# Optimization experiments

Hardware: AMD Instinct MI355X
Metric: run time of the kernel (lower is better)

Reference implementation:

```python
import jax, jax.numpy as jnp
import numpy as np

NUM_HEADS = 16
EPS = 1e-6


def _phi(x):
    # Positive feature map: ELU + 1
    return jax.nn.elu(x) + 1.0


def setup_inputs() -> dict:
    key = jax.random.key(0)
    ks = jax.random.split(key, 5)
    B, L, D = 4, 8192, 1024
    scale = 0.02
    return {
        "x": jax.random.normal(ks[0], (B, L, D), dtype=jnp.float32),
        "Wq": jax.random.normal(ks[1], (D, D), dtype=jnp.float32) * scale,
        "Wk": jax.random.normal(ks[2], (D, D), dtype=jnp.float32) * scale,
        "Wv": jax.random.normal(ks[3], (D, D), dtype=jnp.float32) * scale,
        "Wo": jax.random.normal(ks[4], (D, D), dtype=jnp.float32) * scale,
    }


def reference(x, Wq, Wk, Wv, Wo):
    B, L, D = x.shape
    H = NUM_HEADS
    dh = D // H
    # Projections (bias-free linear layers)
    Q = x @ Wq
    K = x @ Wk
    V = x @ Wv
    # Split heads: (B, H, L, dh)
    Qh = Q.reshape(B, L, H, dh).transpose(0, 2, 1, 3)
    Kh = K.reshape(B, L, H, dh).transpose(0, 2, 1, 3)
    Vh = V.reshape(B, L, H, dh).transpose(0, 2, 1, 3)
    Qf = _phi(Qh)
    Kf = _phi(Kh)
    # Global key-value reduction over time: (B, H, dh, dh)
    Kv = jnp.einsum('bhlm,bhln->bhmn', Kf, Vh)
    # Key normalizer: (B, H, dh)
    K1 = jnp.sum(Kf, axis=2)
    # Numerator / denominator
    num = jnp.einsum('bhlm,bhmn->bhln', Qf, Kv)
    den = jnp.einsum('bhlm,bhm->bhl', Qf, K1) + EPS
    out = num / den[..., None]
    out = out.transpose(0, 2, 1, 3).reshape(B, L, D)
    return out @ Wo
```

## Files before the change

### kernel.cpp

```cpp
#include <hip/hip_runtime.h>
#include <stdint.h>
#include <stddef.h>

typedef __bf16 bf16;
typedef __attribute__((ext_vector_type(8))) __bf16 bf16x8;
typedef __attribute__((ext_vector_type(4))) __bf16 bf16x4;
typedef __attribute__((ext_vector_type(4))) float f32x4;

#define ATT_EPS 1e-6f

__device__ __forceinline__ void lds16(const void* g, void* l) {
    __builtin_amdgcn_global_load_lds(
        (const __attribute__((address_space(1))) void*)g,
        (__attribute__((address_space(3))) void*)l, 16, 0, 0);
}

__global__ __launch_bounds__(256) void cvt_bf16(const float4* __restrict__ in,
                                                bf16x4* __restrict__ out, int n4) {
    int i = blockIdx.x * 256 + threadIdx.x;
    if (i < n4) {
        float4 v = in[i];
        bf16x4 o;
        o.x = (bf16)v.x; o.y = (bf16)v.y; o.z = (bf16)v.z; o.w = (bf16)v.w;
        out[i] = o;
    }
}

__global__ __launch_bounds__(256) void transpose_w(const float* __restrict__ W,
                                                   bf16* __restrict__ Wt) {
    __shared__ float tile[32][33];
    const int bx = blockIdx.x * 32, by = blockIdx.y * 32;
    const int tx = threadIdx.x, ty = threadIdx.y;
#pragma unroll
    for (int j = 0; j < 32; j += 8)
        tile[ty + j][tx] = W[(size_t)(by + ty + j) * 1024 + bx + tx];
    __syncthreads();
#pragma unroll
    for (int j = 0; j < 32; j += 8)
        Wt[(size_t)(bx + ty + j) * 1024 + by + tx] = (bf16)tile[tx][ty + j];
}

template <int MODE>
__global__ __launch_bounds__(256) void gemm_bt(const bf16* __restrict__ A, int lda,
                                               const bf16* __restrict__ B, int ldb,
                                               void* __restrict__ C, int ldc, int K) {
    __shared__ bf16 sA[128 * 32] __attribute__((aligned(16)));
    __shared__ bf16 sB[128 * 32] __attribute__((aligned(16)));
    const int t = threadIdx.x;
    const int wave = t >> 6;
    const int lane = t & 63;
    const int tileM = blockIdx.y * 128;
    const int tileN = blockIdx.x * 128;
    const int wm = (wave >> 1) * 64;
    const int wn = (wave & 1) * 64;

    f32x4 acc[4][4] = {};

    const int srow = t >> 2;
    const int scol = (t & 3) * 8;
    const bf16* a0 = A + (size_t)(tileM + srow) * lda + scol;
    const bf16* a1 = A + (size_t)(tileM + 64 + srow) * lda + scol;
    const bf16* b0 = B + (size_t)(tileN + srow) * ldb + scol;
    const bf16* b1 = B + (size_t)(tileN + 64 + srow) * ldb + scol;
    bf16* dA0 = sA + wave * 512;
    bf16* dA1 = sA + 2048 + wave * 512;
    bf16* dB0 = sB + wave * 512;
    bf16* dB1 = sB + 2048 + wave * 512;

    const int rm = lane & 15;
    const int qk = (lane >> 4) * 8;

    for (int k0 = 0; k0 < K; k0 += 32) {
        lds16(a0 + k0, dA0);
        lds16(a1 + k0, dA1);
        lds16(b0 + k0, dB0);
        lds16(b1 + k0, dB1);
        __builtin_amdgcn_s_waitcnt(0);
        __syncthreads();
        bf16x8 af[4], bfr[4];
#pragma unroll
        for (int mi = 0; mi < 4; mi++)
            af[mi] = *(const bf16x8*)&sA[(wm + mi * 16 + rm) * 32 + qk];
#pragma unroll
        for (int ni = 0; ni < 4; ni++)
            bfr[ni] = *(const bf16x8*)&sB[(wn + ni * 16 + rm) * 32 + qk];
#pragma unroll
        for (int mi = 0; mi < 4; mi++)
#pragma unroll
            for (int ni = 0; ni < 4; ni++)
                acc[mi][ni] = __builtin_amdgcn_mfma_f32_16x16x32_bf16(
                    af[mi], bfr[ni], acc[mi][ni], 0, 0, 0);
        __syncthreads();
    }

    const int row0 = (lane >> 4) * 4;
    const int col = lane & 15;
#pragma unroll
    for (int mi = 0; mi < 4; mi++) {
#pragma unroll
        for (int ni = 0; ni < 4; ni++) {
#pragma unroll
            for (int r = 0; r < 4; r++) {
                int gm = tileM + wm + mi * 16 + row0 + r;
                int gn = tileN + wn + ni * 16 + col;
                float v = acc[mi][ni][r];
                if (MODE == 2) v = (v > 0.f) ? (v + 1.f) : __expf(v);
                if (MODE == 0)
                    ((float*)C)[(size_t)gm * ldc + gn] = v;
                else
                    ((bf16*)C)[(size_t)gm * ldc + gn] = (bf16)v;
            }
        }
    }
}

__global__ __launch_bounds__(256) void kv_reduce(const bf16* __restrict__ Kft,
                                                 const bf16* __restrict__ Vt,
                                                 float* __restrict__ Kv) {
    const int chunk = blockIdx.x;
    const int bh = blockIdx.y;
    const int b = bh >> 4, h = bh & 15;
    __shared__ bf16 sA[64 * 32] __attribute__((aligned(16)));
    __shared__ bf16 sB[64 * 32] __attribute__((aligned(16)));
    const int t = threadIdx.x, wave = t >> 6, lane = t & 63;
    const size_t cbase = (size_t)b * 8192 + (size_t)chunk * 2048;
    const int srow = t >> 2, scol = (t & 3) * 8;
    const bf16* a0 = Kft + (size_t)(h * 64 + srow) * 32768 + cbase + scol;
    const bf16* b0 = Vt + (size_t)(h * 64 + srow) * 32768 + cbase + scol;
    bf16* dA = sA + wave * 512;
    bf16* dB = sB + wave * 512;
    const int rm = lane & 15, qk = (lane >> 4) * 8;

    f32x4 acc[4] = {};
    f32x4 acc1 = {0.f, 0.f, 0.f, 0.f};
    bf16x8 ones;
#pragma unroll
    for (int j = 0; j < 8; j++) ones[j] = (bf16)1.0f;

    for (int k0 = 0; k0 < 2048; k0 += 32) {
        lds16(a0 + k0, dA);
        lds16(b0 + k0, dB);
        __builtin_amdgcn_s_waitcnt(0);
        __syncthreads();
        bf16x8 af = *(const bf16x8*)&sA[(wave * 16 + rm) * 32 + qk];
        bf16x8 bfr[4];
#pragma unroll
        for (int ni = 0; ni < 4; ni++)
            bfr[ni] = *(const bf16x8*)&sB[(ni * 16 + rm) * 32 + qk];
#pragma unroll
        for (int ni = 0; ni < 4; ni++)
            acc[ni] = __builtin_amdgcn_mfma_f32_16x16x32_bf16(af, bfr[ni], acc[ni], 0, 0, 0);
        acc1 = __builtin_amdgcn_mfma_f32_16x16x32_bf16(af, ones, acc1, 0, 0, 0);
        __syncthreads();
    }

    float* out = Kv + bh * 65 * 64;
    const int row0 = (lane >> 4) * 4, col = lane & 15;
    const int m0 = wave * 16 + row0;
#pragma unroll
    for (int ni = 0; ni < 4; ni++)
#pragma unroll
        for (int r = 0; r < 4; r++)
            atomicAdd(&out[(ni * 16 + col) * 64 + m0 + r], acc[ni][r]);
    if (col == 0) {
#pragma unroll
        for (int r = 0; r < 4; r++) atomicAdd(&out[64 * 64 + m0 + r], acc1[r]);
    }
}

__global__ __launch_bounds__(256) void attn_out(const bf16* __restrict__ Qf,
                                                const float* __restrict__ Kv,
                                                bf16* __restrict__ attn) {
    const int lt = blockIdx.x;
    const int bh = blockIdx.y;
    const int b = bh >> 4, h = bh & 15;
    __shared__ bf16 sQ[128 * 64] __attribute__((aligned(16)));
    __shared__ bf16 sB[80 * 64] __attribute__((aligned(16)));
    __shared__ float den[128];
    const int t = threadIdx.x, wave = t >> 6, lane = t & 63;
    const int qrow = t >> 3, qc = (t & 7) * 8;
    const bf16* qp = Qf + (size_t)(b * 8192 + lt * 128 + qrow) * 1024 + h * 64 + qc;
#pragma unroll
    for (int i = 0; i < 4; i++)
        lds16(qp + (size_t)i * 32 * 1024, sQ + i * 2048 + wave * 512);
    const float* kv = Kv + bh * 65 * 64;
    for (int idx = t; idx < 80 * 64; idx += 256) {
        int n = idx >> 6, k2 = idx & 63;
        sB[idx] = (n < 65) ? (bf16)kv[n * 64 + k2] : (bf16)0.f;
    }
    __builtin_amdgcn_s_waitcnt(0);
    __syncthreads();

    f32x4 acc[2][5] = {};
    const int rm = lane & 15, qk = (lane >> 4) * 8;
#pragma unroll
    for (int k0 = 0; k0 < 64; k0 += 32) {
        bf16x8 af[2], bfr[5];
#pragma unroll
        for (int mi = 0; mi < 2; mi++)
            af[mi] = *(const bf16x8*)&sQ[(wave * 32 + mi * 16 + rm) * 64 + k0 + qk];
#pragma unroll
        for (int ni = 0; ni < 5; ni++)
            bfr[ni] = *(const bf16x8*)&sB[(ni * 16 + rm) * 64 + k0 + qk];
#pragma unroll
        for (int mi = 0; mi < 2; mi++)
#pragma unroll
            for (int ni = 0; ni < 5; ni++)
                acc[mi][ni] = __builtin_amdgcn_mfma_f32_16x16x32_bf16(
                    af[mi], bfr[ni], acc[mi][ni], 0, 0, 0);
    }

    const int row0 = (lane >> 4) * 4, col = lane & 15;
    if (col == 0) {
#pragma unroll
        for (int mi = 0; mi < 2; mi++)
#pragma unroll
            for (int r = 0; r < 4; r++)
                den[wave * 32 + mi * 16 + row0 + r] = acc[mi][4][r] + ATT_EPS;
    }
    __syncthreads();
#pragma unroll
    for (int mi = 0; mi < 2; mi++) {
#pragma unroll
        for (int ni = 0; ni < 4; ni++) {
#pragma unroll
            for (int r = 0; r < 4; r++) {
                int rl = wave * 32 + mi * 16 + row0 + r;
                float v = acc[mi][ni][r] / den[rl];
                attn[(size_t)(b * 8192 + lt * 128 + rl) * 1024 + h * 64 + ni * 16 + col] =
                    (bf16)v;
            }
        }
    }
}

extern "C" void kernel_launch(void* const* d_in, const int* in_sizes, int n_in,
                              void* d_out, int out_size, void* d_ws, size_t ws_size,
                              hipStream_t stream) {
    const float* x  = (const float*)d_in[0];
    const float* Wq = (const float*)d_in[1];
    const float* Wk = (const float*)d_in[2];
    const float* Wv = (const float*)d_in[3];
    const float* Wo = (const float*)d_in[4];

    char* ws = (char*)d_ws;
    bf16* xb  = (bf16*)ws;
    bf16* Qf  = (bf16*)(ws + ((size_t)64 << 20));
    bf16* Kft = (bf16*)(ws + ((size_t)128 << 20));
    bf16* Vt  = (bf16*)(ws + ((size_t)192 << 20));
    bf16* Wqt = (bf16*)(ws + ((size_t)256 << 20));
    bf16* Wkt = Wqt + 1024 * 1024;
    bf16* Wvt = Wkt + 1024 * 1024;
    bf16* Wot = Wvt + 1024 * 1024;
    float* Kv = (float*)(Wot + 1024 * 1024);
    bf16* attn = xb;

    cvt_bf16<<<8388608 / 256, 256, 0, stream>>>((const float4*)x, (bf16x4*)xb, 8388608);
    dim3 tb(32, 8);
    transpose_w<<<dim3(32, 32), tb, 0, stream>>>(Wq, Wqt);
    transpose_w<<<dim3(32, 32), tb, 0, stream>>>(Wk, Wkt);
    transpose_w<<<dim3(32, 32), tb, 0, stream>>>(Wv, Wvt);
    transpose_w<<<dim3(32, 32), tb, 0, stream>>>(Wo, Wot);
    hipMemsetAsync(Kv, 0, (size_t)64 * 65 * 64 * sizeof(float), stream);

    gemm_bt<2><<<dim3(8, 256), 256, 0, stream>>>(xb, 1024, Wqt, 1024, Qf, 1024, 1024);
    gemm_bt<2><<<dim3(256, 8), 256, 0, stream>>>(Wkt, 1024, xb, 1024, Kft, 32768, 1024);
    gemm_bt<1><<<dim3(256, 8), 256, 0, stream>>>(Wvt, 1024, xb, 1024, Vt, 32768, 1024);
    kv_reduce<<<dim3(4, 64), 256, 0, stream>>>(Kft, Vt, Kv);
    attn_out<<<dim3(64, 64), 256, 0, stream>>>(Qf, Kv, attn);
    gemm_bt<0><<<dim3(8, 256), 256, 0, stream>>>(attn, 1024, Wot, 1024, d_out, 1024, 1024);
}
```

Baseline: 740.7 us.

## Fuse K and V projections into one GEMM and swizzle tile order

The separate K and V projection GEMMs are merged into a single kernel that loads each x tile once and computes both Wk·x and Wv·x accumulators, with the ELU+1 applied to K in the epilogue. This halves the reads of x for those projections. All GEMMs also switch to a 1D grid with a swizzled block-to-tile mapping, grouping 8 N-tiles per M-group for better L2 reuse. The fused kernel doubles the accumulator registers, so it uses launch_bounds(256,2) and 24KB of LDS, which may reduce occupancy or cause spills.

```diff
diff --git a/kernel.cpp b/kernel.cpp
--- a/kernel.cpp
+++ b/kernel.cpp
@@ -13,6 +13,11 @@
     __builtin_amdgcn_global_load_lds(
         (const __attribute__((address_space(1))) void*)g,
         (__attribute__((address_space(3))) void*)l, 16, 0, 0);
+}
+
+__device__ __forceinline__ void swizzle_uv(int lin, int& u, int& v) {
+    u = (lin & 7) | ((lin >> 6) << 3);
+    v = (lin >> 3) & 7;
 }
 
 __global__ __launch_bounds__(256) void cvt_bf16(const float4* __restrict__ in,
@@ -49,8 +54,10 @@
     const int t = threadIdx.x;
     const int wave = t >> 6;
     const int lane = t & 63;
-    const int tileM = blockIdx.y * 128;
-    const int tileN = blockIdx.x * 128;
+    int u, v;
+    swizzle_uv(blockIdx.x, u, v);
+    const int tileM = u * 128;
+    const int tileN = v * 128;
     const int wm = (wave >> 1) * 64;
     const int wn = (wave & 1) * 64;
 
@@ -103,12 +110,100 @@
             for (int r = 0; r < 4; r++) {
                 int gm = tileM + wm + mi * 16 + row0 + r;
                 int gn = tileN + wn + ni * 16 + col;
-                float v = acc[mi][ni][r];
-                if (MODE == 2) v = (v > 0.f) ? (v + 1.f) : __expf(v);
+                float val = acc[mi][ni][r];
+                if (MODE == 2) val = (val > 0.f) ? (val + 1.f) : __expf(val);
                 if (MODE == 0)
-                    ((float*)C)[(size_t)gm * ldc + gn] = v;
+                    ((float*)C)[(size_t)gm * ldc + gn] = val;
                 else
-                    ((bf16*)C)[(size_t)gm * ldc + gn] = (bf16)v;
+                    ((bf16*)C)[(size_t)gm * ldc + gn] = (bf16)val;
+            }
+        }
+    }
+}
+
+__global__ __launch_bounds__(256, 2) void kv_proj(const bf16* __restrict__ Wkt,
+                                                  const bf16* __restrict__ Wvt,
+                                                  const bf16* __restrict__ xb,
+                                                  bf16* __restrict__ Kft,
+                                                  bf16* __restrict__ Vt) {
+    __shared__ bf16 sK[128 * 32] __attribute__((aligned(16)));
+    __shared__ bf16 sV[128 * 32] __attribute__((aligned(16)));
+    __shared__ bf16 sX[128 * 32] __attribute__((aligned(16)));
+    const int t = threadIdx.x;
+    const int wave = t >> 6;
+    const int lane = t & 63;
+    int u, v;
+    swizzle_uv(blockIdx.x, u, v);
+    const int tileM = v * 128;
+    const int tileN = u * 128;
+    const int wm = (wave >> 1) * 64;
+    const int wn = (wave & 1) * 64;
+
+    f32x4 accK[4][4] = {};
+    f32x4 accV[4][4] = {};
+
+    const int srow = t >> 2;
+    const int scol = (t & 3) * 8;
+    const bf16* k0p = Wkt + (size_t)(tileM + srow) * 1024 + scol;
+    const bf16* k1p = k0p + (size_t)64 * 1024;
+    const bf16* v0p = Wvt + (size_t)(tileM + srow) * 1024 + scol;
+    const bf16* v1p = v0p + (size_t)64 * 1024;
+    const bf16* x0p = xb + (size_t)(tileN + srow) * 1024 + scol;
+    const bf16* x1p = x0p + (size_t)64 * 1024;
+    bf16* dK0 = sK + wave * 512;
+    bf16* dK1 = sK + 2048 + wave * 512;
+    bf16* dV0 = sV + wave * 512;
+    bf16* dV1 = sV + 2048 + wave * 512;
+    bf16* dX0 = sX + wave * 512;
+    bf16* dX1 = sX + 2048 + wave * 512;
+
+    const int rm = lane & 15;
+    const int qk = (lane >> 4) * 8;
+
+    for (int k0 = 0; k0 < 1024; k0 += 32) {
+        lds16(k0p + k0, dK0);
+        lds16(k1p + k0, dK1);
+        lds16(v0p + k0, dV0);
+        lds16(v1p + k0, dV1);
+        lds16(x0p + k0, dX0);
+        lds16(x1p + k0, dX1);
+        __builtin_amdgcn_s_waitcnt(0);
+        __syncthreads();
+        bf16x8 bfr[4], afK[4], afV[4];
+#pragma unroll
+        for (int ni = 0; ni < 4; ni++)
+            bfr[ni] = *(const bf16x8*)&sX[(wn + ni * 16 + rm) * 32 + qk];
+#pragma unroll
+        for (int mi = 0; mi < 4; mi++) {
+            afK[mi] = *(const bf16x8*)&sK[(wm + mi * 16 + rm) * 32 + qk];
+            afV[mi] = *(const bf16x8*)&sV[(wm + mi * 16 + rm) * 32 + qk];
+        }
+#pragma unroll
+        for (int mi = 0; mi < 4; mi++)
+#pragma unroll
+            for (int ni = 0; ni < 4; ni++) {
+                accK[mi][ni] = __builtin_amdgcn_mfma_f32_16x16x32_bf16(
+                    afK[mi], bfr[ni], accK[mi][ni], 0, 0, 0);
+                accV[mi][ni] = __builtin_amdgcn_mfma_f32_16x16x32_bf16(
+                    afV[mi], bfr[ni], accV[mi][ni], 0, 0, 0);
+            }
+        __syncthreads();
+    }
+
+    const int row0 = (lane >> 4) * 4;
+    const int col = lane & 15;
+#pragma unroll
+    for (int mi = 0; mi < 4; mi++) {
+#pragma unroll
+        for (int ni = 0; ni < 4; ni++) {
+#pragma unroll
+            for (int r = 0; r < 4; r++) {
+                int gm = tileM + wm + mi * 16 + row0 + r;
+                int gn = tileN + wn + ni * 16 + col;
+                float kv_ = accK[mi][ni][r];
+                kv_ = (kv_ > 0.f) ? (kv_ + 1.f) : __expf(kv_);
+                Kft[(size_t)gm * 32768 + gn] = (bf16)kv_;
+                Vt[(size_t)gm * 32768 + gn] = (bf16)accV[mi][ni][r];
             }
         }
     }
@@ -226,9 +321,9 @@
 #pragma unroll
             for (int r = 0; r < 4; r++) {
                 int rl = wave * 32 + mi * 16 + row0 + r;
-                float v = acc[mi][ni][r] / den[rl];
+                float vv = acc[mi][ni][r] / den[rl];
                 attn[(size_t)(b * 8192 + lt * 128 + rl) * 1024 + h * 64 + ni * 16 + col] =
-                    (bf16)v;
+                    (bf16)vv;
             }
         }
     }
@@ -263,10 +358,9 @@
     transpose_w<<<dim3(32, 32), tb, 0, stream>>>(Wo, Wot);
     hipMemsetAsync(Kv, 0, (size_t)64 * 65 * 64 * sizeof(float), stream);
 
-    gemm_bt<2><<<dim3(8, 256), 256, 0, stream>>>(xb, 1024, Wqt, 1024, Qf, 1024, 1024);
-    gemm_bt<2><<<dim3(256, 8), 256, 0, stream>>>(Wkt, 1024, xb, 1024, Kft, 32768, 1024);
-    gemm_bt<1><<<dim3(256, 8), 256, 0, stream>>>(Wvt, 1024, xb, 1024, Vt, 32768, 1024);
+    gemm_bt<2><<<2048, 256, 0, stream>>>(xb, 1024, Wqt, 1024, Qf, 1024, 1024);
+    kv_proj<<<2048, 256, 0, stream>>>(Wkt, Wvt, xb, Kft, Vt);
     kv_reduce<<<dim3(4, 64), 256, 0, stream>>>(Kft, Vt, Kv);
     attn_out<<<dim3(64, 64), 256, 0, stream>>>(Qf, Kv, attn);
-    gemm_bt<0><<<dim3(8, 256), 256, 0, stream>>>(attn, 1024, Wot, 1024, d_out, 1024, 1024);
-}
+    gemm_bt<0><<<2048, 256, 0, stream>>>(attn, 1024, Wot, 1024, d_out, 1024, 1024);
+}
```

Result: faster. 705.4 us (-4.8%).
